# Performance work log

Measured on AMD Instinct MI355X. Metric: run time of the kernel, lower is better.

The kernel has to match this reference:

```python
import jax, jax.numpy as jnp
import numpy as np

IGNORE_INDEX = -100


def setup_inputs() -> dict:
    key = jax.random.key(0)
    k1, k2, k3 = jax.random.split(key, 3)
    BT, H, V = 4096, 2048, 32000
    hidden_states = jax.random.normal(k1, (BT, H), dtype=jnp.float32) * 0.02
    weight = jax.random.normal(k2, (V, H), dtype=jnp.float32) * 0.02
    targets = jax.random.randint(k3, (BT,), 0, V, dtype=jnp.int64)
    return {"hidden_states": hidden_states, "weight": weight, "targets": targets}


def reference(hidden_states, weight, targets):
    # Fused lm_head projection + cross-entropy with ignore_index masking,
    # 'mean' reduction over valid rows (matches reduction='mean').
    logits = jnp.einsum('bh,vh->bv', hidden_states, weight).astype(jnp.float32)  # (BT, V)
    lse = jax.nn.logsumexp(logits, axis=-1)  # (BT,)
    safe_tgt = jnp.clip(targets, 0, logits.shape[-1] - 1)
    target_logit = jnp.take_along_axis(logits, safe_tgt[:, None], axis=-1)[:, 0]
    valid = targets != IGNORE_INDEX
    loss_rows = jnp.where(valid, lse - target_logit, 0.0)  # (BT,)
    n_valid = jnp.maximum(valid.sum(), 1)
    return loss_rows.sum() / n_valid.astype(jnp.float32)
```

## Files before the change

kernel.cpp:

```cpp
#include <hip/hip_runtime.h>

#define BT 4096
#define H  2048
#define V  32000
#define BM 256
#define BN 128
#define BKB 128
#define KT (H / BKB)
#define NTILES (V / BN)
#define MTILES (BT / BM)
#define NWG (MTILES * NTILES)
#define IGNORE_INDEX (-100)

typedef int   v8i   __attribute__((ext_vector_type(8)));
typedef float f32x4 __attribute__((ext_vector_type(4)));

#define SCALE_ONE 0x7F7F7F7F
#define UNSCALE   (1.0f / 65536.0f)

#define BAR()   __builtin_amdgcn_s_barrier()
#define SB0()   __builtin_amdgcn_sched_barrier(0)
#define LGKM0() asm volatile("s_waitcnt lgkmcnt(0)" ::: "memory")
#define VMC(N)  asm volatile("s_waitcnt vmcnt(" #N ")" ::: "memory")

__device__ inline void load_lds16(const void* g, void* l) {
  __builtin_amdgcn_global_load_lds(
      (const __attribute__((address_space(1))) unsigned int*)g,
      (__attribute__((address_space(3))) unsigned int*)l,
      16, 0, 0);
}

__global__ __launch_bounds__(256)
void cvt_pack_kernel(const float* __restrict__ in, unsigned char* __restrict__ out,
                     int tasks) {
  __shared__ float ld[4][16][132];
  const int wv = threadIdx.x >> 6, lane = threadIdx.x & 63;
  const int task = blockIdx.x * 4 + wv;
  if (task >= tasks) return;
  const int g = task >> 4, kt = task & 15;
  const float* src = in + (size_t)(g * 16) * H + kt * 128;
#pragma unroll
  for (int i = 0; i < 8; ++i) {
    int idx = i * 64 + lane;
    int r = idx >> 5, c = idx & 31;
    float4 v = *(const float4*)(src + (size_t)r * H + c * 4);
    *(float4*)&ld[wv][r][c * 4] = v;
  }
  LGKM0();
  const int row = lane & 15, kb = (lane >> 4) * 32;
  int p[8];
#pragma unroll
  for (int u = 0; u < 8; ++u) {
    float4 x = *(const float4*)&ld[wv][row][kb + u * 4];
    int v = 0;
    v = __builtin_amdgcn_cvt_pk_fp8_f32(x.x * 256.f, x.y * 256.f, v, false);
    v = __builtin_amdgcn_cvt_pk_fp8_f32(x.z * 256.f, x.w * 256.f, v, true);
    p[u] = v;
  }
  unsigned char* dst = out + ((size_t)g * KT + kt) * 2048 + lane * 16;
  int4 lo; lo.x = p[0]; lo.y = p[1]; lo.z = p[2]; lo.w = p[3];
  int4 hi; hi.x = p[4]; hi.y = p[5]; hi.z = p[6]; hi.w = p[7];
  *(int4*)dst          = lo;
  *(int4*)(dst + 1024) = hi;
}

union frag_u { v8i v; int4 h[2]; };

#define MF(C, A, B)                                                         \
  (C) = __builtin_amdgcn_mfma_scale_f32_16x16x128_f8f6f4(                   \
      (A).v, (B).v, (C), 0, 0, 0, SCALE_ONE, 0, SCALE_ONE)

__global__ __launch_bounds__(512, 2)
void gemm_lse_kernel(const unsigned char* __restrict__ Af8,
                     const unsigned char* __restrict__ Bf8,
                     const int* __restrict__ tgt,
                     float* __restrict__ pm, float* __restrict__ pl,
                     float* __restrict__ tl) {
  __shared__ __align__(16) unsigned char As[2 * 32768];
  __shared__ __align__(16) unsigned char Bs[2 * 16384];
  __shared__ float red_m[2][BM];
  __shared__ float red_l[2][BM];
  __shared__ int   stgt[BM];

  const int wgid = ((int)blockIdx.x & 7) * (NWG / 8) + ((int)blockIdx.x >> 3);
  const int mt = wgid & (MTILES - 1);
  const int nt = wgid >> 4;
  const int m0 = mt * BM;
  const int n0 = nt * BN;

  const int tid  = threadIdx.x;
  const int lane = tid & 63;
  const int w    = tid >> 6;
  const int wr   = w >> 1;
  const int wc   = w & 1;
  const int lm   = lane & 15;
  const int q    = lane >> 4;

  if (tid < BM) stgt[tid] = tgt[m0 + tid];
  __syncthreads();

  const unsigned char* aSrc = Af8 + (size_t)(m0 / 16) * KT * 2048;
  const unsigned char* bSrc = Bf8 + (size_t)(n0 / 16) * KT * 2048;

  auto stage = [&](int buf, int kt) {
#pragma unroll
    for (int e = 0; e < 2; ++e) {
      const int g = 2 * w + e;
      const unsigned char* s = aSrc + ((size_t)g * KT + kt) * 2048;
      unsigned char* d = As + buf * 32768 + g * 2048;
      load_lds16(s, d);
      load_lds16(s + 1024, d + 1024);
    }
    const unsigned char* s = bSrc + ((size_t)w * KT + kt) * 2048;
    unsigned char* d = Bs + buf * 16384 + w * 2048;
    load_lds16(s, d);
    load_lds16(s + 1024, d + 1024);
  };

  const unsigned char* aRd = As + (wr * 4) * 2048 + lane * 16;
  const unsigned char* bRd = Bs + (wc * 4) * 2048 + lane * 16;

  auto ldA = [&](frag_u& f, int buf, int i) {
    const unsigned char* p = aRd + buf * 32768 + i * 2048;
    f.h[0] = *(const int4*)(p);
    f.h[1] = *(const int4*)(p + 1024);
  };
  auto ldB = [&](frag_u& f, int buf, int j) {
    const unsigned char* p = bRd + buf * 16384 + j * 2048;
    f.h[0] = *(const int4*)(p);
    f.h[1] = *(const int4*)(p + 1024);
  };

  f32x4 acc[4][4];
#pragma unroll
  for (int a = 0; a < 4; ++a)
#pragma unroll
    for (int b = 0; b < 4; ++b) acc[a][b] = (f32x4){0.f, 0.f, 0.f, 0.f};

  frag_u faX[4], fbX[4], faY[4], fbY[4];

#define LDSET(SET, BUF)                                                     \
  ldA(fa##SET[0], BUF, 0); ldA(fa##SET[1], BUF, 1);                         \
  ldA(fa##SET[2], BUF, 2); ldA(fa##SET[3], BUF, 3);                         \
  ldB(fb##SET[0], BUF, 0); ldB(fb##SET[1], BUF, 1);                         \
  ldB(fb##SET[2], BUF, 2); ldB(fb##SET[3], BUF, 3);

#define MFSET(SET)                                                          \
  __builtin_amdgcn_s_setprio(1);                                            \
  MF(acc[0][0], fa##SET[0], fb##SET[0]); MF(acc[1][0], fa##SET[1], fb##SET[0]); \
  MF(acc[2][0], fa##SET[2], fb##SET[0]); MF(acc[3][0], fa##SET[3], fb##SET[0]); \
  MF(acc[0][1], fa##SET[0], fb##SET[1]); MF(acc[1][1], fa##SET[1], fb##SET[1]); \
  MF(acc[2][1], fa##SET[2], fb##SET[1]); MF(acc[3][1], fa##SET[3], fb##SET[1]); \
  MF(acc[0][2], fa##SET[0], fb##SET[2]); MF(acc[1][2], fa##SET[1], fb##SET[2]); \
  MF(acc[2][2], fa##SET[2], fb##SET[2]); MF(acc[3][2], fa##SET[3], fb##SET[2]); \
  MF(acc[0][3], fa##SET[0], fb##SET[3]); MF(acc[1][3], fa##SET[1], fb##SET[3]); \
  MF(acc[2][3], fa##SET[2], fb##SET[3]); MF(acc[3][3], fa##SET[3], fb##SET[3]); \
  __builtin_amdgcn_s_setprio(0);

  stage(0, 0);
  VMC(0); SB0(); BAR(); SB0();
  stage(1, 1);
  LDSET(X, 0)
  LGKM0(); VMC(0); SB0(); BAR(); SB0();

  for (int it = 0; it < 8; ++it) {
    const bool pre = (it < 7);

    if (pre) stage(0, 2 * it + 2);
    LDSET(Y, 1)
    MFSET(X)
    LGKM0(); VMC(0); SB0(); BAR(); SB0();

    if (pre) {
      stage(1, 2 * it + 3);
      LDSET(X, 0)
    }
    MFSET(Y)
    LGKM0(); VMC(0); SB0(); BAR(); SB0();
  }

  __syncthreads();

#pragma unroll
  for (int ai = 0; ai < 4; ++ai) {
#pragma unroll
    for (int r = 0; r < 4; ++r) {
      int row_local = wr * 64 + ai * 16 + q * 4 + r;
      int c = stgt[row_local] - n0 - wc * 64;
      if ((unsigned)c < 64u && (c & 15) == lm) {
        int bj = c >> 4;
        float v = bj == 0 ? acc[ai][0][r]
                : bj == 1 ? acc[ai][1][r]
                : bj == 2 ? acc[ai][2][r]
                :           acc[ai][3][r];
        tl[m0 + row_local] = v * UNSCALE;
      }
    }
  }

#pragma unroll
  for (int ai = 0; ai < 4; ++ai) {
#pragma unroll
    for (int r = 0; r < 4; ++r) {
      float v0 = acc[ai][0][r] * UNSCALE;
      float v1 = acc[ai][1][r] * UNSCALE;
      float v2 = acc[ai][2][r] * UNSCALE;
      float v3 = acc[ai][3][r] * UNSCALE;
      float mx = fmaxf(fmaxf(v0, v1), fmaxf(v2, v3));
#pragma unroll
      for (int off = 1; off < 16; off <<= 1) mx = fmaxf(mx, __shfl_xor(mx, off));
      float s = __expf(v0 - mx) + __expf(v1 - mx) + __expf(v2 - mx) + __expf(v3 - mx);
#pragma unroll
      for (int off = 1; off < 16; off <<= 1) s += __shfl_xor(s, off);
      if (lm == 0) {
        int row_local = wr * 64 + ai * 16 + q * 4 + r;
        red_m[wc][row_local] = mx;
        red_l[wc][row_local] = s;
      }
    }
  }
  __syncthreads();
  if (tid < BM) {
    float ma = red_m[0][tid], mb = red_m[1][tid];
    float M = fmaxf(ma, mb);
    float L = red_l[0][tid] * __expf(ma - M) + red_l[1][tid] * __expf(mb - M);
    long idx = (long)nt * BT + (m0 + tid);
    pm[idx] = M;
    pl[idx] = L;
  }
}

__global__ __launch_bounds__(256)
void row_lse_kernel(const float* __restrict__ pm, const float* __restrict__ pl,
                    const float* __restrict__ tl, const int* __restrict__ tgt,
                    float* __restrict__ rl) {
  int row  = blockIdx.x * 4 + (threadIdx.x >> 6);
  int lane = threadIdx.x & 63;
  float M = -__builtin_inff();
  float L = 0.f;
  for (int t = lane; t < NTILES; t += 64) {
    float m2 = pm[(long)t * BT + row];
    float l2 = pl[(long)t * BT + row];
    float Mn = fmaxf(M, m2);
    L = L * __expf(M - Mn) + l2 * __expf(m2 - Mn);
    M = Mn;
  }
#pragma unroll
  for (int off = 1; off < 64; off <<= 1) {
    float m2 = __shfl_xor(M, off);
    float l2 = __shfl_xor(L, off);
    float Mn = fmaxf(M, m2);
    L = L * __expf(M - Mn) + l2 * __expf(m2 - Mn);
    M = Mn;
  }
  if (lane == 0) {
    float lse = M + logf(L);
    int t = tgt[row];
    rl[row] = (t != IGNORE_INDEX) ? (lse - tl[row]) : 0.f;
  }
}

__global__ __launch_bounds__(256)
void final_kernel(const float* __restrict__ rl, const int* __restrict__ tgt,
                  float* __restrict__ out) {
  __shared__ float ss[4];
  __shared__ float sc[4];
  float s = 0.f, c = 0.f;
  for (int r = threadIdx.x; r < BT; r += 256) {
    s += rl[r];
    c += (tgt[r] != IGNORE_INDEX) ? 1.f : 0.f;
  }
#pragma unroll
  for (int off = 32; off > 0; off >>= 1) {
    s += __shfl_xor(s, off);
    c += __shfl_xor(c, off);
  }
  int w = threadIdx.x >> 6;
  if ((threadIdx.x & 63) == 0) { ss[w] = s; sc[w] = c; }
  __syncthreads();
  if (threadIdx.x == 0) {
    float S = ss[0] + ss[1] + ss[2] + ss[3];
    float C = sc[0] + sc[1] + sc[2] + sc[3];
    out[0] = S / fmaxf(C, 1.f);
  }
}

extern "C" void kernel_launch(void* const* d_in, const int* in_sizes, int n_in,
                              void* d_out, int out_size, void* d_ws, size_t ws_size,
                              hipStream_t stream) {
  const float* hs  = (const float*)d_in[0];
  const float* wt  = (const float*)d_in[1];
  const int*   tgt = (const int*)d_in[2];
  float*       out = (float*)d_out;

  char* ws = (char*)d_ws;
  size_t off = 0;
  auto alloc = [&](size_t bytes) -> void* {
    void* p = ws + off;
    off += (bytes + 255) & ~(size_t)255;
    return p;
  };
  unsigned char* wf8 = (unsigned char*)alloc((size_t)V * H);
  unsigned char* hf8 = (unsigned char*)alloc((size_t)BT * H);
  float* pm = (float*)alloc((size_t)NTILES * BT * 4);
  float* pl = (float*)alloc((size_t)NTILES * BT * 4);
  float* tl = (float*)alloc((size_t)BT * 4);
  float* rl = (float*)alloc((size_t)BT * 4);
  (void)ws_size; (void)in_sizes; (void)n_in; (void)out_size;

  cvt_pack_kernel<<<(V / 16) * KT / 4, 256, 0, stream>>>(wt, wf8, (V / 16) * KT);
  cvt_pack_kernel<<<(BT / 16) * KT / 4, 256, 0, stream>>>(hs, hf8, (BT / 16) * KT);

  gemm_lse_kernel<<<NWG, 512, 0, stream>>>(hf8, wf8, tgt, pm, pl, tl);

  row_lse_kernel<<<BT / 4, 256, 0, stream>>>(pm, pl, tl, tgt, rl);
  final_kernel<<<1, 256, 0, stream>>>(rl, tgt, out);
}
```

Before: 817.2 us.

## Shrink GEMM tile to 128x128 with 256 threads and fuse small kernels

Halves the M tile of the fused FP8 GEMM+LSE kernel (BM 256 to 128) and drops the workgroup to 4 waves. This doubles the number of workgroups and roughly halves LDS per block, to improve occupancy and load balance. It also merges the two convert launches into one and folds the final reduction into the row-LSE kernel using atomics plus a last-block-done counter, which removes launch overhead. The smaller tile lowers A/B reuse per block, so more global and L2 traffic goes to the weight operand.

```diff
diff --git a/kernel.cpp b/kernel.cpp
--- a/kernel.cpp
+++ b/kernel.cpp
@@ -3,7 +3,7 @@
 #define BT 4096
 #define H  2048
 #define V  32000
-#define BM 256
+#define BM 128
 #define BN 128
 #define BKB 128
 #define KT (H / BKB)
@@ -30,13 +30,24 @@
       16, 0, 0);
 }
 
+#define W_TASKS ((V / 16) * KT)
+#define H_TASKS ((BT / 16) * KT)
 __global__ __launch_bounds__(256)
-void cvt_pack_kernel(const float* __restrict__ in, unsigned char* __restrict__ out,
-                     int tasks) {
+void cvt_pack_kernel(const float* __restrict__ wt, const float* __restrict__ hs,
+                     unsigned char* __restrict__ wf8, unsigned char* __restrict__ hf8,
+                     float* __restrict__ accbuf) {
+  if (blockIdx.x == 0 && threadIdx.x == 0) {
+    accbuf[0] = 0.f;
+    accbuf[1] = 0.f;
+    ((unsigned*)accbuf)[2] = 0u;
+  }
   __shared__ float ld[4][16][132];
   const int wv = threadIdx.x >> 6, lane = threadIdx.x & 63;
-  const int task = blockIdx.x * 4 + wv;
-  if (task >= tasks) return;
+  int task = blockIdx.x * 4 + wv;
+  if (task >= W_TASKS + H_TASKS) return;
+  const float* in = wt;
+  unsigned char* out = wf8;
+  if (task >= W_TASKS) { task -= W_TASKS; in = hs; out = hf8; }
   const int g = task >> 4, kt = task & 15;
   const float* src = in + (size_t)(g * 16) * H + kt * 128;
 #pragma unroll
@@ -70,13 +81,13 @@
   (C) = __builtin_amdgcn_mfma_scale_f32_16x16x128_f8f6f4(                   \
       (A).v, (B).v, (C), 0, 0, 0, SCALE_ONE, 0, SCALE_ONE)
 
-__global__ __launch_bounds__(512, 2)
+__global__ __launch_bounds__(256, 2)
 void gemm_lse_kernel(const unsigned char* __restrict__ Af8,
                      const unsigned char* __restrict__ Bf8,
                      const int* __restrict__ tgt,
                      float* __restrict__ pm, float* __restrict__ pl,
                      float* __restrict__ tl) {
-  __shared__ __align__(16) unsigned char As[2 * 32768];
+  __shared__ __align__(16) unsigned char As[2 * 16384];
   __shared__ __align__(16) unsigned char Bs[2 * 16384];
   __shared__ float red_m[2][BM];
   __shared__ float red_l[2][BM];
@@ -84,7 +95,7 @@
 
   const int wgid = ((int)blockIdx.x & 7) * (NWG / 8) + ((int)blockIdx.x >> 3);
   const int mt = wgid & (MTILES - 1);
-  const int nt = wgid >> 4;
+  const int nt = wgid >> 5;
   const int m0 = mt * BM;
   const int n0 = nt * BN;
 
@@ -106,22 +117,22 @@
 #pragma unroll
     for (int e = 0; e < 2; ++e) {
       const int g = 2 * w + e;
-      const unsigned char* s = aSrc + ((size_t)g * KT + kt) * 2048;
-      unsigned char* d = As + buf * 32768 + g * 2048;
-      load_lds16(s, d);
-      load_lds16(s + 1024, d + 1024);
-    }
-    const unsigned char* s = bSrc + ((size_t)w * KT + kt) * 2048;
-    unsigned char* d = Bs + buf * 16384 + w * 2048;
-    load_lds16(s, d);
-    load_lds16(s + 1024, d + 1024);
+      const unsigned char* sa = aSrc + ((size_t)g * KT + kt) * 2048;
+      unsigned char* da = As + buf * 16384 + g * 2048;
+      load_lds16(sa, da);
+      load_lds16(sa + 1024, da + 1024);
+      const unsigned char* sb = bSrc + ((size_t)g * KT + kt) * 2048;
+      unsigned char* db = Bs + buf * 16384 + g * 2048;
+      load_lds16(sb, db);
+      load_lds16(sb + 1024, db + 1024);
+    }
   };
 
   const unsigned char* aRd = As + (wr * 4) * 2048 + lane * 16;
   const unsigned char* bRd = Bs + (wc * 4) * 2048 + lane * 16;
 
   auto ldA = [&](frag_u& f, int buf, int i) {
-    const unsigned char* p = aRd + buf * 32768 + i * 2048;
+    const unsigned char* p = aRd + buf * 16384 + i * 2048;
     f.h[0] = *(const int4*)(p);
     f.h[1] = *(const int4*)(p + 1024);
   };
@@ -231,10 +242,12 @@
 }
 
 __global__ __launch_bounds__(256)
-void row_lse_kernel(const float* __restrict__ pm, const float* __restrict__ pl,
-                    const float* __restrict__ tl, const int* __restrict__ tgt,
-                    float* __restrict__ rl) {
-  int row  = blockIdx.x * 4 + (threadIdx.x >> 6);
+void rowlse_final_kernel(const float* __restrict__ pm, const float* __restrict__ pl,
+                         const float* __restrict__ tl, const int* __restrict__ tgt,
+                         float* __restrict__ accbuf, float* __restrict__ out) {
+  __shared__ float sl[4], sc2[4];
+  int wv   = threadIdx.x >> 6;
+  int row  = blockIdx.x * 4 + wv;
   int lane = threadIdx.x & 63;
   float M = -__builtin_inff();
   float L = 0.f;
@@ -254,34 +267,22 @@
     M = Mn;
   }
   if (lane == 0) {
-    float lse = M + logf(L);
     int t = tgt[row];
-    rl[row] = (t != IGNORE_INDEX) ? (lse - tl[row]) : 0.f;
-  }
-}
-
-__global__ __launch_bounds__(256)
-void final_kernel(const float* __restrict__ rl, const int* __restrict__ tgt,
-                  float* __restrict__ out) {
-  __shared__ float ss[4];
-  __shared__ float sc[4];
-  float s = 0.f, c = 0.f;
-  for (int r = threadIdx.x; r < BT; r += 256) {
-    s += rl[r];
-    c += (tgt[r] != IGNORE_INDEX) ? 1.f : 0.f;
-  }
-#pragma unroll
-  for (int off = 32; off > 0; off >>= 1) {
-    s += __shfl_xor(s, off);
-    c += __shfl_xor(c, off);
-  }
-  int w = threadIdx.x >> 6;
-  if ((threadIdx.x & 63) == 0) { ss[w] = s; sc[w] = c; }
+    bool valid = (t != IGNORE_INDEX);
+    sl[wv]  = valid ? (M + logf(L) - tl[row]) : 0.f;
+    sc2[wv] = valid ? 1.f : 0.f;
+  }
   __syncthreads();
   if (threadIdx.x == 0) {
-    float S = ss[0] + ss[1] + ss[2] + ss[3];
-    float C = sc[0] + sc[1] + sc[2] + sc[3];
-    out[0] = S / fmaxf(C, 1.f);
+    atomicAdd(&accbuf[0], sl[0] + sl[1] + sl[2] + sl[3]);
+    atomicAdd(&accbuf[1], sc2[0] + sc2[1] + sc2[2] + sc2[3]);
+    __threadfence();
+    unsigned t = atomicAdd((unsigned*)accbuf + 2, 1u);
+    if (t == gridDim.x - 1) {
+      float S = atomicAdd(&accbuf[0], 0.f);
+      float C = atomicAdd(&accbuf[1], 0.f);
+      out[0] = S / fmaxf(C, 1.f);
+    }
   }
 }
 
@@ -305,14 +306,10 @@
   float* pm = (float*)alloc((size_t)NTILES * BT * 4);
   float* pl = (float*)alloc((size_t)NTILES * BT * 4);
   float* tl = (float*)alloc((size_t)BT * 4);
-  float* rl = (float*)alloc((size_t)BT * 4);
+  float* accbuf = (float*)alloc(256);
   (void)ws_size; (void)in_sizes; (void)n_in; (void)out_size;
 
-  cvt_pack_kernel<<<(V / 16) * KT / 4, 256, 0, stream>>>(wt, wf8, (V / 16) * KT);
-  cvt_pack_kernel<<<(BT / 16) * KT / 4, 256, 0, stream>>>(hs, hf8, (BT / 16) * KT);
-
-  gemm_lse_kernel<<<NWG, 512, 0, stream>>>(hf8, wf8, tgt, pm, pl, tl);
-
-  row_lse_kernel<<<BT / 4, 256, 0, stream>>>(pm, pl, tl, tgt, rl);
-  final_kernel<<<1, 256, 0, stream>>>(rl, tgt, out);
-}
+  cvt_pack_kernel<<<(W_TASKS + H_TASKS) / 4, 256, 0, stream>>>(wt, hs, wf8, hf8, accbuf);
+  gemm_lse_kernel<<<NWG, 256, 0, stream>>>(hf8, wf8, tgt, pm, pl, tl);
+  rowlse_final_kernel<<<BT / 4, 256, 0, stream>>>(pm, pl, tl, tgt, accbuf, out);
+}
```

Result: no change. 822.2 us (+0.6%).
